# Kernel optimization log

Measured on AMD Instinct MI355X. Metric: run time of the kernel, lower is better.

The kernel has to match this reference:

```python
import jax, jax.numpy as jnp
import numpy as np

N = 50000   # num_entities
E = 600000  # num_edges
D = 128     # dim
R = 200     # num_relations
T = 1000    # num_timestamps
L = 2       # num_layers


def setup_inputs() -> dict:
    key = jax.random.key(0)
    ks = jax.random.split(key, 16)
    edge_index = jax.random.randint(ks[0], (2, E), 0, N)
    edge_type = jax.random.randint(ks[1], (E,), 0, R)
    edge_time = jax.random.randint(ks[2], (E,), 0, T)
    edge_weight = jax.random.uniform(ks[3], (E,), dtype=jnp.float32)
    perm = jax.random.permutation(ks[4], N)
    entity_emb = jax.random.normal(ks[5], (N, D), dtype=jnp.float32)
    rel_emb = jax.random.normal(ks[6], (R, D), dtype=jnp.float32)
    time_emb = jax.random.normal(ks[7], (T, D), dtype=jnp.float32)
    s = 1.0 / np.sqrt(D)
    in_proj_w = jax.random.uniform(ks[8], (L, D, 2 * D), minval=-s, maxval=s)
    in_proj_b = jax.random.uniform(ks[9], (L, 2 * D), minval=-s, maxval=s)
    out_proj_w = jax.random.uniform(ks[10], (L, D, D), minval=-s, maxval=s)
    out_proj_b = jax.random.uniform(ks[11], (L, D), minval=-s, maxval=s)
    A = jax.random.normal(ks[12], (L, D)) * 0.1
    B = jax.random.normal(ks[13], (L, D)) * 0.1
    ln_g = jnp.ones((L, D), dtype=jnp.float32)
    ln_b = jnp.zeros((L, D), dtype=jnp.float32)
    return dict(edge_index=edge_index, edge_type=edge_type, edge_time=edge_time,
                edge_weight=edge_weight, perm=perm, entity_emb=entity_emb,
                rel_emb=rel_emb, time_emb=time_emb, in_proj_w=in_proj_w,
                in_proj_b=in_proj_b, out_proj_w=out_proj_w, out_proj_b=out_proj_b,
                A=A, B=B, ln_g=ln_g, ln_b=ln_b)


def _mamba_layer(x, Wi, bi, Wo, bo, A, B, g_ln, b_ln):
    # x: [N, D]
    zg = x @ Wi + bi                      # [N, 2D]
    z, g = jnp.split(zg, 2, axis=-1)
    g = jax.nn.sigmoid(g)

    def step(prev, zg_i):
        z_i, g_i = zg_i
        curr = g_i * (A * prev) + B * z_i
        return curr, curr

    _, h = jax.lax.scan(step, jnp.zeros((D,), x.dtype), (z, g))  # [N, D]
    y = x + h @ Wo + bo
    mu = jnp.mean(y, axis=-1, keepdims=True)
    var = jnp.mean((y - mu) ** 2, axis=-1, keepdims=True)
    return (y - mu) / jnp.sqrt(var + 1e-5) * g_ln + b_ln


def reference(edge_index, edge_type, edge_time, edge_weight, perm, entity_emb,
              rel_emb, time_emb, in_proj_w, in_proj_b, out_proj_w, out_proj_b,
              A, B, ln_g, ln_b):
    src, dst = edge_index[0], edge_index[1]
    msgs = entity_emb[src] + rel_emb[edge_type] + time_emb[edge_time]  # [E, D]
    sums = jax.ops.segment_sum(msgs * edge_weight[:, None], dst, num_segments=N)
    cnt = jax.ops.segment_sum(edge_weight, dst, num_segments=N)
    x = sums / jnp.maximum(cnt, 1.0)[:, None]          # scatter_mean
    x = x / jnp.maximum(jnp.linalg.norm(x, axis=1, keepdims=True), 1e-12)
    x = x[perm]
    for l in range(L):
        x = _mamba_layer(x, in_proj_w[l], in_proj_b[l], out_proj_w[l],
                         out_proj_b[l], A[l], B[l], ln_g[l], ln_b[l])
    return x
```

## Files before the change

kernel.cpp:

```cpp
#include <hip/hip_runtime.h>
#include <hip/hip_bf16.h>

typedef unsigned short ushort_t;
typedef unsigned int   uint_t;
typedef __attribute__((ext_vector_type(8))) short bf8;
typedef __attribute__((ext_vector_type(4))) float f32x4;

constexpr int N = 50000;
constexpr int E = 600000;
constexpr int D = 128;
constexpr int L = 2;
constexpr int NB = (N + 255) / 256;

constexpr int TR   = 48;
constexpr int LOOK = 16;
constexpr int NBLK = (N + TR - 1) / TR;
constexpr int HSTR = 136;

__device__ __forceinline__ float us2f(ushort_t u) {
    union { uint_t i; float f; } c; c.i = (uint_t)u << 16; return c.f;
}
__device__ __forceinline__ ushort_t f2us(float f) {
    __hip_bfloat16 b = __float2bfloat16(f);
    return *(ushort_t*)&b;
}

__global__ __launch_bounds__(256) void k_hist(
    const int* __restrict__ dstp, int* __restrict__ hist)
{
    int e = blockIdx.x * 256 + threadIdx.x;
    if (e < E) atomicAdd(&hist[dstp[e]], 1);
}

__global__ __launch_bounds__(256) void k_scan1(
    const int* __restrict__ hist, int* __restrict__ part, int* __restrict__ bsum)
{
    int i = blockIdx.x * 256 + threadIdx.x;
    int v = (i < N) ? hist[i] : 0;
    int lane = threadIdx.x & 63, wv = threadIdx.x >> 6;
    int s = v;
    #pragma unroll
    for (int m = 1; m < 64; m <<= 1) {
        int t = __shfl_up(s, m, 64);
        if (lane >= m) s += t;
    }
    __shared__ int wsum[4];
    if (lane == 63) wsum[wv] = s;
    __syncthreads();
    int off = 0;
    for (int w = 0; w < wv; w++) off += wsum[w];
    if (i < N) part[i] = s - v + off;
    if (threadIdx.x == 255)
        bsum[blockIdx.x] = wsum[0] + wsum[1] + wsum[2] + wsum[3];
}

__global__ __launch_bounds__(256) void k_scan2(int* __restrict__ bsum)
{
    int i = threadIdx.x;
    int v = (i < NB) ? bsum[i] : 0;
    int lane = i & 63, wv = i >> 6;
    int s = v;
    #pragma unroll
    for (int m = 1; m < 64; m <<= 1) {
        int t = __shfl_up(s, m, 64);
        if (lane >= m) s += t;
    }
    __shared__ int wsum[4];
    if (lane == 63) wsum[wv] = s;
    __syncthreads();
    int off = 0;
    for (int w = 0; w < wv; w++) off += wsum[w];
    if (i < NB) bsum[i] = s - v + off;
}

__global__ __launch_bounds__(256) void k_finalize(
    const int* __restrict__ part, const int* __restrict__ bsum,
    int* __restrict__ cursor, int* __restrict__ rowst,
    const int* __restrict__ perm, int* __restrict__ invp)
{
    int i = blockIdx.x * 256 + threadIdx.x;
    if (i < N) {
        int b = part[i] + bsum[i >> 8];
        cursor[i] = b;
        rowst[i] = b;
        invp[perm[i]] = i;
    }
}

__global__ __launch_bounds__(256) void k_scatter(
    const int* __restrict__ eidx, const int* __restrict__ etype,
    const int* __restrict__ etime, const float* __restrict__ ew,
    int* __restrict__ cursor, int2* __restrict__ esort)
{
    int e = blockIdx.x * 256 + threadIdx.x;
    if (e >= E) return;
    int dst = eidx[E + e];
    int slot = atomicAdd(&cursor[dst], 1);
    int2 p;
    p.x = (eidx[e] & 0xffff) | (etype[e] << 16);
    p.y = (etime[e] & 0xffff) | ((int)f2us(ew[e]) << 16);
    esort[slot] = p;
}

__global__ __launch_bounds__(256) void k_cast(
    const float* __restrict__ ent, const float* __restrict__ rel,
    const float* __restrict__ tim, const float* __restrict__ Wi,
    const float* __restrict__ Wo, ushort_t* __restrict__ entb,
    ushort_t* __restrict__ relb, ushort_t* __restrict__ timb,
    ushort_t* __restrict__ WiT, ushort_t* __restrict__ WoT)
{
    size_t t = (size_t)blockIdx.x * 256 + threadIdx.x;
    if (t < 3276800) {
        const float2* s; uint_t* d; size_t off;
        if (t < 3200000)      { s = (const float2*)ent; d = (uint_t*)entb; off = t; }
        else if (t < 3212800) { s = (const float2*)rel; d = (uint_t*)relb; off = t - 3200000; }
        else                  { s = (const float2*)tim; d = (uint_t*)timb; off = t - 3212800; }
        float2 v = s[off];
        d[off] = (uint_t)f2us(v.x) | ((uint_t)f2us(v.y) << 16);
    } else {
        size_t u = t - 3276800;
        if (u < (size_t)L * 256 * 128) {
            int l = u / (256 * 128), r = u % (256 * 128);
            int n = r / 128, k = r % 128;
            WiT[u] = f2us(Wi[(size_t)l * 128 * 256 + k * 256 + n]);
        } else if (u < (size_t)L * 256 * 128 + L * 128 * 128) {
            size_t v = u - (size_t)L * 256 * 128;
            int l = v / (128 * 128), r = v % (128 * 128);
            int n = r / 128, k = r % 128;
            WoT[v] = f2us(Wo[(size_t)l * 128 * 128 + k * 128 + n]);
        }
    }
}

__global__ __launch_bounds__(256) void k_agg(
    const int2* __restrict__ esort, const int* __restrict__ rowst,
    const int* __restrict__ hist, const int* __restrict__ invp,
    const ushort_t* __restrict__ entb, const ushort_t* __restrict__ relb,
    const ushort_t* __restrict__ timb, ushort_t* __restrict__ xbf)
{
    int wv = threadIdx.x >> 6, lane = threadIdx.x & 63;
    int d = blockIdx.x * 4 + wv;
    if (d >= N) return;
    int beg = rowst[d];
    int n = hist[d];

    float s0[4] = {0.f, 0.f, 0.f, 0.f};
    float s1[4] = {0.f, 0.f, 0.f, 0.f};
    float sw[4] = {0.f, 0.f, 0.f, 0.f};

    int j = 0;
    for (; j + 3 < n; j += 4) {
        int2 rec[4];
        #pragma unroll
        for (int u = 0; u < 4; u++) rec[u] = esort[beg + j + u];
        #pragma unroll
        for (int u = 0; u < 4; u++) {
            int  sA = rec[u].x & 0xffff, tA = ((uint_t)rec[u].x) >> 16;
            int  mA = rec[u].y & 0xffff;
            float w = us2f((ushort_t)(((uint_t)rec[u].y) >> 16));
            uint_t va = *(const uint_t*)(entb + (size_t)sA * D + 2 * lane);
            uint_t vb = *(const uint_t*)(relb + (size_t)tA * D + 2 * lane);
            uint_t vc = *(const uint_t*)(timb + (size_t)mA * D + 2 * lane);
            s0[u] += (us2f(va & 0xffff) + us2f(vb & 0xffff) + us2f(vc & 0xffff)) * w;
            s1[u] += (us2f(va >> 16)    + us2f(vb >> 16)    + us2f(vc >> 16))    * w;
            sw[u] += w;
        }
    }
    for (; j < n; j++) {
        int2 p = esort[beg + j];
        int  sA = p.x & 0xffff, tA = ((uint_t)p.x) >> 16;
        int  mA = p.y & 0xffff;
        float w = us2f((ushort_t)(((uint_t)p.y) >> 16));
        uint_t va = *(const uint_t*)(entb + (size_t)sA * D + 2 * lane);
        uint_t vb = *(const uint_t*)(relb + (size_t)tA * D + 2 * lane);
        uint_t vc = *(const uint_t*)(timb + (size_t)mA * D + 2 * lane);
        s0[0] += (us2f(va & 0xffff) + us2f(vb & 0xffff) + us2f(vc & 0xffff)) * w;
        s1[0] += (us2f(va >> 16)    + us2f(vb >> 16)    + us2f(vc >> 16))    * w;
        sw[0] += w;
    }
    float a0 = (s0[0] + s0[1]) + (s0[2] + s0[3]);
    float a1 = (s1[0] + s1[1]) + (s1[2] + s1[3]);
    float wsum = (sw[0] + sw[1]) + (sw[2] + sw[3]);

    float inv = 1.0f / fmaxf(wsum, 1.0f);
    a0 *= inv; a1 *= inv;

    float ss = a0 * a0 + a1 * a1;
    #pragma unroll
    for (int m = 32; m >= 1; m >>= 1) ss += __shfl_xor(ss, m, 64);
    float sc = 1.0f / fmaxf(sqrtf(ss), 1e-12f);

    int orow = invp[d];
    uint_t out = (uint_t)f2us(a0 * sc) | ((uint_t)f2us(a1 * sc) << 16);
    *(uint_t*)(xbf + (size_t)orow * D + 2 * lane) = out;
}

template <bool FINAL>
__global__ __launch_bounds__(256, 4) void k_layer(
    const ushort_t* __restrict__ xin, const ushort_t* __restrict__ WiT,
    const float* __restrict__ bi, const ushort_t* __restrict__ WoT,
    const float* __restrict__ bo, const float* __restrict__ Aw,
    const float* __restrict__ Bw, const float* __restrict__ lg,
    const float* __restrict__ lb, ushort_t* __restrict__ xoutb,
    float* __restrict__ outf)
{
    __shared__ ushort_t hs[TR * HSTR];
    __shared__ float redS[TR * 4], redQ[TR * 4], muA[TR], rsA[TR];

    int tid = threadIdx.x;
    int w = tid >> 6, lane = tid & 63;
    int quad = lane >> 4, m = lane & 15;
    int r0 = blockIdx.x * TR;
    int base = r0 - LOOK;

    const bf8 zero8 = {0, 0, 0, 0, 0, 0, 0, 0};
    const f32x4 zero4 = {0.f, 0.f, 0.f, 0.f};

    int cz0 = w * 32 + m;
    int cz1 = cz0 + 16;

    float Ad0 = Aw[cz0], Bd0 = Bw[cz0];
    float Ad1 = Aw[cz1], Bd1 = Bw[cz1];
    float bz0 = bi[cz0], bz1 = bi[cz1];
    float bg0 = bi[cz0 + 128], bg1 = bi[cz1 + 128];

    bf8 Bz0[4], Bz1[4], Bg0[4], Bg1[4];
    {
        int colz0 = w * 32 + m, colz1 = colz0 + 16;
        #pragma unroll
        for (int kb = 0; kb < 4; kb++) {
            int ko = kb * 32 + quad * 8;
            Bz0[kb] = *(const bf8*)(WiT + (size_t)colz0 * 128 + ko);
            Bz1[kb] = *(const bf8*)(WiT + (size_t)colz1 * 128 + ko);
            Bg0[kb] = *(const bf8*)(WiT + (size_t)(colz0 + 128) * 128 + ko);
            Bg1[kb] = *(const bf8*)(WiT + (size_t)(colz1 + 128) * 128 + ko);
        }
    }

    float carry0 = 0.f, carry1 = 0.f;
    for (int rt = 0; rt < 4; rt++) {
        int gr = base + rt * 16 + m;
        bf8 a[4];
        if (gr >= 0 && gr < N) {
            #pragma unroll
            for (int kb = 0; kb < 4; kb++)
                a[kb] = *(const bf8*)(xin + (size_t)gr * 128 + kb * 32 + quad * 8);
        } else {
            #pragma unroll
            for (int kb = 0; kb < 4; kb++) a[kb] = zero8;
        }
        f32x4 az0 = zero4, az1 = zero4, ag0 = zero4, ag1 = zero4;
        #pragma unroll
        for (int kb = 0; kb < 4; kb++) {
            az0 = __builtin_amdgcn_mfma_f32_16x16x32_bf16(a[kb], Bz0[kb], az0, 0, 0, 0);
            az1 = __builtin_amdgcn_mfma_f32_16x16x32_bf16(a[kb], Bz1[kb], az1, 0, 0, 0);
            ag0 = __builtin_amdgcn_mfma_f32_16x16x32_bf16(a[kb], Bg0[kb], ag0, 0, 0, 0);
            ag1 = __builtin_amdgcn_mfma_f32_16x16x32_bf16(a[kb], Bg1[kb], ag1, 0, 0, 0);
        }
        float P0 = 1.f, Q0 = 0.f, P1 = 1.f, Q1 = 0.f;
        #pragma unroll
        for (int reg = 0; reg < 4; reg++) {
            int grr = base + rt * 16 + quad * 4 + reg;
            bool ok = (grr >= 0) && (grr < N);
            float z0 = az0[reg] + bz0, z1 = az1[reg] + bz1;
            float g0 = 1.f / (1.f + __expf(-(ag0[reg] + bg0)));
            float g1 = 1.f / (1.f + __expf(-(ag1[reg] + bg1)));
            float ca0 = ok ? g0 * Ad0 : 0.f, cb0 = ok ? Bd0 * z0 : 0.f;
            float ca1 = ok ? g1 * Ad1 : 0.f, cb1 = ok ? Bd1 * z1 : 0.f;
            az0[reg] = ca0; ag0[reg] = cb0;
            az1[reg] = ca1; ag1[reg] = cb1;
            P0 = ca0 * P0; Q0 = ca0 * Q0 + cb0;
            P1 = ca1 * P1; Q1 = ca1 * Q1 + cb1;
        }
        float Pp, Qp;
        Pp = __shfl_up(P0, 16, 64); Qp = __shfl_up(Q0, 16, 64);
        if (quad >= 1) { Q0 = P0 * Qp + Q0; P0 = P0 * Pp; }
        Pp = __shfl_up(P1, 16, 64); Qp = __shfl_up(Q1, 16, 64);
        if (quad >= 1) { Q1 = P1 * Qp + Q1; P1 = P1 * Pp; }
        Pp = __shfl_up(P0, 32, 64); Qp = __shfl_up(Q0, 32, 64);
        if (quad >= 2) { Q0 = P0 * Qp + Q0; P0 = P0 * Pp; }
        Pp = __shfl_up(P1, 32, 64); Qp = __shfl_up(Q1, 32, 64);
        if (quad >= 2) { Q1 = P1 * Qp + Q1; P1 = P1 * Pp; }
        float Pe0 = __shfl_up(P0, 16, 64), Qe0 = __shfl_up(Q0, 16, 64);
        float Pe1 = __shfl_up(P1, 16, 64), Qe1 = __shfl_up(Q1, 16, 64);
        if (quad == 0) { Pe0 = 1.f; Qe0 = 0.f; Pe1 = 1.f; Qe1 = 0.f; }
        float h0 = Pe0 * carry0 + Qe0;
        float h1 = Pe1 * carry1 + Qe1;
        float Pc0 = __shfl(P0, m + 48, 64), Qc0 = __shfl(Q0, m + 48, 64);
        float Pc1 = __shfl(P1, m + 48, 64), Qc1 = __shfl(Q1, m + 48, 64);
        carry0 = Pc0 * carry0 + Qc0;
        carry1 = Pc1 * carry1 + Qc1;
        #pragma unroll
        for (int reg = 0; reg < 4; reg++) {
            h0 = az0[reg] * h0 + ag0[reg];
            h1 = az1[reg] * h1 + ag1[reg];
            if (rt >= 1) {
                int lrow = (rt - 1) * 16 + quad * 4 + reg;
                hs[lrow * HSTR + cz0] = f2us(h0);
                hs[lrow * HSTR + cz1] = f2us(h1);
            }
        }
    }
    __syncthreads();

    float y[3][2][4];
    {
        int c0 = w * 32 + m, c1 = c0 + 16;
        float bias0 = bo[c0], bias1 = bo[c1];
        bf8 b0[4], b1[4];
        #pragma unroll
        for (int kb = 0; kb < 4; kb++) {
            int ko = kb * 32 + quad * 8;
            b0[kb] = *(const bf8*)(WoT + (size_t)c0 * 128 + ko);
            b1[kb] = *(const bf8*)(WoT + (size_t)c1 * 128 + ko);
        }
        #pragma unroll
        for (int rt = 0; rt < 3; rt++) {
            bf8 a[4];
            #pragma unroll
            for (int kb = 0; kb < 4; kb++)
                a[kb] = *(const bf8*)(hs + (rt * 16 + m) * HSTR + kb * 32 + quad * 8);
            f32x4 acc0 = zero4, acc1 = zero4;
            #pragma unroll
            for (int kb = 0; kb < 4; kb++) {
                acc0 = __builtin_amdgcn_mfma_f32_16x16x32_bf16(a[kb], b0[kb], acc0, 0, 0, 0);
                acc1 = __builtin_amdgcn_mfma_f32_16x16x32_bf16(a[kb], b1[kb], acc1, 0, 0, 0);
            }
            #pragma unroll
            for (int reg = 0; reg < 4; reg++) {
                int gr = r0 + rt * 16 + quad * 4 + reg;
                float r0v = 0.f, r1v = 0.f;
                if (gr < N) {
                    r0v = us2f(xin[(size_t)gr * 128 + c0]);
                    r1v = us2f(xin[(size_t)gr * 128 + c1]);
                }
                y[rt][0][reg] = acc0[reg] + bias0 + r0v;
                y[rt][1][reg] = acc1[reg] + bias1 + r1v;
            }
        }
    }

    {
        #pragma unroll
        for (int rt = 0; rt < 3; rt++)
            #pragma unroll
            for (int reg = 0; reg < 4; reg++) {
                float v0 = y[rt][0][reg], v1 = y[rt][1][reg];
                float s = v0 + v1, q = v0 * v0 + v1 * v1;
                #pragma unroll
                for (int mk = 1; mk <= 8; mk <<= 1) {
                    s += __shfl_xor(s, mk, 64);
                    q += __shfl_xor(q, mk, 64);
                }
                if (m == 0) {
                    int row = rt * 16 + quad * 4 + reg;
                    redS[row * 4 + w] = s;
                    redQ[row * 4 + w] = q;
                }
            }
    }
    __syncthreads();
    if (tid < TR) {
        float s = redS[tid * 4] + redS[tid * 4 + 1] + redS[tid * 4 + 2] + redS[tid * 4 + 3];
        float q = redQ[tid * 4] + redQ[tid * 4 + 1] + redQ[tid * 4 + 2] + redQ[tid * 4 + 3];
        float mu = s * (1.f / 128.f);
        float var = q * (1.f / 128.f) - mu * mu;
        muA[tid] = mu;
        rsA[tid] = rsqrtf(var + 1e-5f);
    }
    __syncthreads();
    {
        int c0 = w * 32 + m, c1 = c0 + 16;
        float gl0 = lg[c0], gl1 = lg[c1], bl0 = lb[c0], bl1 = lb[c1];
        #pragma unroll
        for (int rt = 0; rt < 3; rt++)
            #pragma unroll
            for (int reg = 0; reg < 4; reg++) {
                int rr = rt * 16 + quad * 4 + reg;
                int gr = r0 + rr;
                if (gr < N) {
                    float mu = muA[rr], rs = rsA[rr];
                    float v0 = (y[rt][0][reg] - mu) * rs * gl0 + bl0;
                    float v1 = (y[rt][1][reg] - mu) * rs * gl1 + bl1;
                    if (FINAL) {
                        outf[(size_t)gr * 128 + c0] = v0;
                        outf[(size_t)gr * 128 + c1] = v1;
                    } else {
                        xoutb[(size_t)gr * 128 + c0] = f2us(v0);
                        xoutb[(size_t)gr * 128 + c1] = f2us(v1);
                    }
                }
            }
    }
}

extern "C" void kernel_launch(void* const* d_in, const int* in_sizes, int n_in,
                              void* d_out, int out_size, void* d_ws, size_t ws_size,
                              hipStream_t stream)
{
    const int*   eidx  = (const int*)d_in[0];
    const int*   etype = (const int*)d_in[1];
    const int*   etime = (const int*)d_in[2];
    const float* ew    = (const float*)d_in[3];
    const int*   perm  = (const int*)d_in[4];
    const float* ent   = (const float*)d_in[5];
    const float* rel   = (const float*)d_in[6];
    const float* tim   = (const float*)d_in[7];
    const float* Wi    = (const float*)d_in[8];
    const float* bi    = (const float*)d_in[9];
    const float* Wo    = (const float*)d_in[10];
    const float* bo    = (const float*)d_in[11];
    const float* Aw    = (const float*)d_in[12];
    const float* Bw    = (const float*)d_in[13];
    const float* lg    = (const float*)d_in[14];
    const float* lbp   = (const float*)d_in[15];

    char* base = (char*)d_ws;
    size_t o = 0;
    ushort_t* xbf  = (ushort_t*)(base + o); o += (size_t)N * D * 2;
    ushort_t* xb2  = (ushort_t*)(base + o); o += (size_t)N * D * 2;
    ushort_t* entb = (ushort_t*)(base + o); o += (size_t)N * D * 2;
    ushort_t* relb = (ushort_t*)(base + o); o += (size_t)200 * D * 2;
    ushort_t* timb = (ushort_t*)(base + o); o += (size_t)1000 * D * 2;
    ushort_t* WiT  = (ushort_t*)(base + o); o += (size_t)L * 256 * 128 * 2;
    ushort_t* WoT  = (ushort_t*)(base + o); o += (size_t)L * 128 * 128 * 2;
    int2*     esort  = (int2*)(base + o);   o += (size_t)E * 8;
    int*      hist   = (int*)(base + o);    o += (size_t)N * 4;
    int*      part   = (int*)(base + o);    o += (size_t)N * 4;
    int*      bsum   = (int*)(base + o);    o += 256 * 4;
    int*      cursor = (int*)(base + o);    o += (size_t)N * 4;
    int*      rowst  = (int*)(base + o);    o += (size_t)N * 4;
    int*      invp   = (int*)(base + o);    o += (size_t)N * 4;

    hipMemsetAsync(hist, 0, N * sizeof(int), stream);

    k_cast    <<<13185, 256, 0, stream>>>(ent, rel, tim, Wi, Wo,
                                          entb, relb, timb, WiT, WoT);
    k_hist    <<<(E + 255) / 256, 256, 0, stream>>>(eidx + E, hist);
    k_scan1   <<<NB, 256, 0, stream>>>(hist, part, bsum);
    k_scan2   <<<1, 256, 0, stream>>>(bsum);
    k_finalize<<<NB, 256, 0, stream>>>(part, bsum, cursor, rowst, perm, invp);
    k_scatter <<<(E + 255) / 256, 256, 0, stream>>>(eidx, etype, etime, ew,
                                                    cursor, esort);
    k_agg     <<<(N + 3) / 4, 256, 0, stream>>>(esort, rowst, hist, invp,
                                                entb, relb, timb, xbf);

    k_layer<false><<<NBLK, 256, 0, stream>>>(
        xbf, WiT, bi, WoT, bo, Aw, Bw, lg, lbp, xb2, nullptr);
    k_layer<true><<<NBLK, 256, 0, stream>>>(
        xb2, WiT + (size_t)256 * 128, bi + 256, WoT + (size_t)128 * 128,
        bo + 128, Aw + 128, Bw + 128, lg + 128, lbp + 128,
        nullptr, (float*)d_out);
}
```

Baseline: 304.6 us.

## Split mamba layer into coefficient GEMM kernel and scan+output kernel

Each layer is split into two kernels. The first computes the gate and z projections once per row and stores packed bf16 scan coefficients to global memory. The second runs a sequential lookback scan over those coefficients per channel with 128 threads, then applies the out-projection, residual and layernorm on 16-row blocks. This removes the redundant lookback GEMM that the fused 48-row tiles did, at the cost of an extra global round trip for the coefficient buffer, two extra launches, and a serial scan with few active threads.

```diff
diff --git a/kernel.cpp b/kernel.cpp
--- a/kernel.cpp
+++ b/kernel.cpp
@@ -12,9 +12,9 @@
 constexpr int L = 2;
 constexpr int NB = (N + 255) / 256;
 
-constexpr int TR   = 48;
+constexpr int RB   = 16;
+constexpr int RBLK = N / RB;
 constexpr int LOOK = 16;
-constexpr int NBLK = (N + TR - 1) / TR;
 constexpr int HSTR = 136;
 
 __device__ __forceinline__ float us2f(ushort_t u) {
@@ -195,26 +195,15 @@
     *(uint_t*)(xbf + (size_t)orow * D + 2 * lane) = out;
 }
 
-template <bool FINAL>
-__global__ __launch_bounds__(256, 4) void k_layer(
+__global__ __launch_bounds__(256, 4) void k_zg(
     const ushort_t* __restrict__ xin, const ushort_t* __restrict__ WiT,
-    const float* __restrict__ bi, const ushort_t* __restrict__ WoT,
-    const float* __restrict__ bo, const float* __restrict__ Aw,
-    const float* __restrict__ Bw, const float* __restrict__ lg,
-    const float* __restrict__ lb, ushort_t* __restrict__ xoutb,
-    float* __restrict__ outf)
-{
-    __shared__ ushort_t hs[TR * HSTR];
-    __shared__ float redS[TR * 4], redQ[TR * 4], muA[TR], rsA[TR];
-
+    const float* __restrict__ bi, const float* __restrict__ Aw,
+    const float* __restrict__ Bw, uint_t* __restrict__ coeff)
+{
     int tid = threadIdx.x;
     int w = tid >> 6, lane = tid & 63;
     int quad = lane >> 4, m = lane & 15;
-    int r0 = blockIdx.x * TR;
-    int base = r0 - LOOK;
-
-    const bf8 zero8 = {0, 0, 0, 0, 0, 0, 0, 0};
-    const f32x4 zero4 = {0.f, 0.f, 0.f, 0.f};
+    int r0 = blockIdx.x * RB;
 
     int cz0 = w * 32 + m;
     int cz1 = cz0 + 16;
@@ -224,143 +213,139 @@
     float bz0 = bi[cz0], bz1 = bi[cz1];
     float bg0 = bi[cz0 + 128], bg1 = bi[cz1 + 128];
 
+    const f32x4 zero4 = {0.f, 0.f, 0.f, 0.f};
+
     bf8 Bz0[4], Bz1[4], Bg0[4], Bg1[4];
+    #pragma unroll
+    for (int kb = 0; kb < 4; kb++) {
+        int ko = kb * 32 + quad * 8;
+        Bz0[kb] = *(const bf8*)(WiT + (size_t)cz0 * 128 + ko);
+        Bz1[kb] = *(const bf8*)(WiT + (size_t)cz1 * 128 + ko);
+        Bg0[kb] = *(const bf8*)(WiT + (size_t)(cz0 + 128) * 128 + ko);
+        Bg1[kb] = *(const bf8*)(WiT + (size_t)(cz1 + 128) * 128 + ko);
+    }
+
+    bf8 a[4];
+    #pragma unroll
+    for (int kb = 0; kb < 4; kb++)
+        a[kb] = *(const bf8*)(xin + (size_t)(r0 + m) * 128 + kb * 32 + quad * 8);
+
+    f32x4 az0 = zero4, az1 = zero4, ag0 = zero4, ag1 = zero4;
+    #pragma unroll
+    for (int kb = 0; kb < 4; kb++) {
+        az0 = __builtin_amdgcn_mfma_f32_16x16x32_bf16(a[kb], Bz0[kb], az0, 0, 0, 0);
+        az1 = __builtin_amdgcn_mfma_f32_16x16x32_bf16(a[kb], Bz1[kb], az1, 0, 0, 0);
+        ag0 = __builtin_amdgcn_mfma_f32_16x16x32_bf16(a[kb], Bg0[kb], ag0, 0, 0, 0);
+        ag1 = __builtin_amdgcn_mfma_f32_16x16x32_bf16(a[kb], Bg1[kb], ag1, 0, 0, 0);
+    }
+
+    #pragma unroll
+    for (int reg = 0; reg < 4; reg++) {
+        int row = r0 + quad * 4 + reg;
+        float z0 = az0[reg] + bz0, z1 = az1[reg] + bz1;
+        float g0 = 1.f / (1.f + __expf(-(ag0[reg] + bg0)));
+        float g1 = 1.f / (1.f + __expf(-(ag1[reg] + bg1)));
+        uint_t c0 = (uint_t)f2us(g0 * Ad0) | ((uint_t)f2us(Bd0 * z0) << 16);
+        uint_t c1 = (uint_t)f2us(g1 * Ad1) | ((uint_t)f2us(Bd1 * z1) << 16);
+        coeff[(size_t)row * 128 + cz0] = c0;
+        coeff[(size_t)row * 128 + cz1] = c1;
+    }
+}
+
+template <bool FINAL>
+__global__ __launch_bounds__(256, 4) void k_scanout(
+    const uint_t* __restrict__ coeff, const ushort_t* __restrict__ xin,
+    const ushort_t* __restrict__ WoT, const float* __restrict__ bo,
+    const float* __restrict__ lg, const float* __restrict__ lb,
+    ushort_t* __restrict__ xoutb, float* __restrict__ outf)
+{
+    __shared__ ushort_t hs[RB * HSTR];
+    __shared__ float redS[RB * 4], redQ[RB * 4], muA[RB], rsA[RB];
+
+    int tid = threadIdx.x;
+    int w = tid >> 6, lane = tid & 63;
+    int quad = lane >> 4, m = lane & 15;
+    int r0 = blockIdx.x * RB;
+
+    int c0 = w * 32 + m, c1 = c0 + 16;
+
+    bf8 b0[4], b1[4];
+    #pragma unroll
+    for (int kb = 0; kb < 4; kb++) {
+        int ko = kb * 32 + quad * 8;
+        b0[kb] = *(const bf8*)(WoT + (size_t)c0 * 128 + ko);
+        b1[kb] = *(const bf8*)(WoT + (size_t)c1 * 128 + ko);
+    }
+    float bias0 = bo[c0], bias1 = bo[c1];
+    float gl0 = lg[c0], gl1 = lg[c1], bl0 = lb[c0], bl1 = lb[c1];
+
+    float r0v[4], r1v[4];
+    #pragma unroll
+    for (int reg = 0; reg < 4; reg++) {
+        int gr = r0 + quad * 4 + reg;
+        r0v[reg] = us2f(xin[(size_t)gr * 128 + c0]);
+        r1v[reg] = us2f(xin[(size_t)gr * 128 + c1]);
+    }
+
+    if (tid < 128) {
+        float h = 0.f;
+        int rbase = r0 - LOOK;
+        #pragma unroll
+        for (int i = 0; i < LOOK; i++) {
+            int row = rbase + i;
+            int rc = row < 0 ? 0 : row;
+            uint_t c = coeff[(size_t)rc * 128 + tid];
+            float ca = us2f((ushort_t)(c & 0xffff));
+            float cb = us2f((ushort_t)(c >> 16));
+            h = (row >= 0) ? fmaf(ca, h, cb) : 0.f;
+        }
+        #pragma unroll
+        for (int i = 0; i < RB; i++) {
+            uint_t c = coeff[(size_t)(r0 + i) * 128 + tid];
+            float ca = us2f((ushort_t)(c & 0xffff));
+            float cb = us2f((ushort_t)(c >> 16));
+            h = fmaf(ca, h, cb);
+            hs[i * HSTR + tid] = f2us(h);
+        }
+    }
+    __syncthreads();
+
+    float y[2][4];
     {
-        int colz0 = w * 32 + m, colz1 = colz0 + 16;
+        bf8 a[4];
+        #pragma unroll
+        for (int kb = 0; kb < 4; kb++)
+            a[kb] = *(const bf8*)(hs + m * HSTR + kb * 32 + quad * 8);
+        f32x4 acc0 = {0.f, 0.f, 0.f, 0.f}, acc1 = acc0;
         #pragma unroll
         for (int kb = 0; kb < 4; kb++) {
-            int ko = kb * 32 + quad * 8;
-            Bz0[kb] = *(const bf8*)(WiT + (size_t)colz0 * 128 + ko);
-            Bz1[kb] = *(const bf8*)(WiT + (size_t)colz1 * 128 + ko);
-            Bg0[kb] = *(const bf8*)(WiT + (size_t)(colz0 + 128) * 128 + ko);
-            Bg1[kb] = *(const bf8*)(WiT + (size_t)(colz1 + 128) * 128 + ko);
-        }
-    }
-
-    float carry0 = 0.f, carry1 = 0.f;
-    for (int rt = 0; rt < 4; rt++) {
-        int gr = base + rt * 16 + m;
-        bf8 a[4];
-        if (gr >= 0 && gr < N) {
-            #pragma unroll
-            for (int kb = 0; kb < 4; kb++)
-                a[kb] = *(const bf8*)(xin + (size_t)gr * 128 + kb * 32 + quad * 8);
-        } else {
-            #pragma unroll
-            for (int kb = 0; kb < 4; kb++) a[kb] = zero8;
-        }
-        f32x4 az0 = zero4, az1 = zero4, ag0 = zero4, ag1 = zero4;
-        #pragma unroll
-        for (int kb = 0; kb < 4; kb++) {
-            az0 = __builtin_amdgcn_mfma_f32_16x16x32_bf16(a[kb], Bz0[kb], az0, 0, 0, 0);
-            az1 = __builtin_amdgcn_mfma_f32_16x16x32_bf16(a[kb], Bz1[kb], az1, 0, 0, 0);
-            ag0 = __builtin_amdgcn_mfma_f32_16x16x32_bf16(a[kb], Bg0[kb], ag0, 0, 0, 0);
-            ag1 = __builtin_amdgcn_mfma_f32_16x16x32_bf16(a[kb], Bg1[kb], ag1, 0, 0, 0);
-        }
-        float P0 = 1.f, Q0 = 0.f, P1 = 1.f, Q1 = 0.f;
+            acc0 = __builtin_amdgcn_mfma_f32_16x16x32_bf16(a[kb], b0[kb], acc0, 0, 0, 0);
+            acc1 = __builtin_amdgcn_mfma_f32_16x16x32_bf16(a[kb], b1[kb], acc1, 0, 0, 0);
+        }
         #pragma unroll
         for (int reg = 0; reg < 4; reg++) {
-            int grr = base + rt * 16 + quad * 4 + reg;
-            bool ok = (grr >= 0) && (grr < N);
-            float z0 = az0[reg] + bz0, z1 = az1[reg] + bz1;
-            float g0 = 1.f / (1.f + __expf(-(ag0[reg] + bg0)));
-            float g1 = 1.f / (1.f + __expf(-(ag1[reg] + bg1)));
-            float ca0 = ok ? g0 * Ad0 : 0.f, cb0 = ok ? Bd0 * z0 : 0.f;
-            float ca1 = ok ? g1 * Ad1 : 0.f, cb1 = ok ? Bd1 * z1 : 0.f;
-            az0[reg] = ca0; ag0[reg] = cb0;
-            az1[reg] = ca1; ag1[reg] = cb1;
-            P0 = ca0 * P0; Q0 = ca0 * Q0 + cb0;
-            P1 = ca1 * P1; Q1 = ca1 * Q1 + cb1;
-        }
-        float Pp, Qp;
-        Pp = __shfl_up(P0, 16, 64); Qp = __shfl_up(Q0, 16, 64);
-        if (quad >= 1) { Q0 = P0 * Qp + Q0; P0 = P0 * Pp; }
-        Pp = __shfl_up(P1, 16, 64); Qp = __shfl_up(Q1, 16, 64);
-        if (quad >= 1) { Q1 = P1 * Qp + Q1; P1 = P1 * Pp; }
-        Pp = __shfl_up(P0, 32, 64); Qp = __shfl_up(Q0, 32, 64);
-        if (quad >= 2) { Q0 = P0 * Qp + Q0; P0 = P0 * Pp; }
-        Pp = __shfl_up(P1, 32, 64); Qp = __shfl_up(Q1, 32, 64);
-        if (quad >= 2) { Q1 = P1 * Qp + Q1; P1 = P1 * Pp; }
-        float Pe0 = __shfl_up(P0, 16, 64), Qe0 = __shfl_up(Q0, 16, 64);
-        float Pe1 = __shfl_up(P1, 16, 64), Qe1 = __shfl_up(Q1, 16, 64);
-        if (quad == 0) { Pe0 = 1.f; Qe0 = 0.f; Pe1 = 1.f; Qe1 = 0.f; }
-        float h0 = Pe0 * carry0 + Qe0;
-        float h1 = Pe1 * carry1 + Qe1;
-        float Pc0 = __shfl(P0, m + 48, 64), Qc0 = __shfl(Q0, m + 48, 64);
-        float Pc1 = __shfl(P1, m + 48, 64), Qc1 = __shfl(Q1, m + 48, 64);
-        carry0 = Pc0 * carry0 + Qc0;
-        carry1 = Pc1 * carry1 + Qc1;
-        #pragma unroll
-        for (int reg = 0; reg < 4; reg++) {
-            h0 = az0[reg] * h0 + ag0[reg];
-            h1 = az1[reg] * h1 + ag1[reg];
-            if (rt >= 1) {
-                int lrow = (rt - 1) * 16 + quad * 4 + reg;
-                hs[lrow * HSTR + cz0] = f2us(h0);
-                hs[lrow * HSTR + cz1] = f2us(h1);
-            }
+            y[0][reg] = acc0[reg] + bias0 + r0v[reg];
+            y[1][reg] = acc1[reg] + bias1 + r1v[reg];
+        }
+    }
+
+    #pragma unroll
+    for (int reg = 0; reg < 4; reg++) {
+        float v0 = y[0][reg], v1 = y[1][reg];
+        float s = v0 + v1, q = v0 * v0 + v1 * v1;
+        #pragma unroll
+        for (int mk = 1; mk <= 8; mk <<= 1) {
+            s += __shfl_xor(s, mk, 64);
+            q += __shfl_xor(q, mk, 64);
+        }
+        if (m == 0) {
+            int row = quad * 4 + reg;
+            redS[row * 4 + w] = s;
+            redQ[row * 4 + w] = q;
         }
     }
     __syncthreads();
-
-    float y[3][2][4];
-    {
-        int c0 = w * 32 + m, c1 = c0 + 16;
-        float bias0 = bo[c0], bias1 = bo[c1];
-        bf8 b0[4], b1[4];
-        #pragma unroll
-        for (int kb = 0; kb < 4; kb++) {
-            int ko = kb * 32 + quad * 8;
-            b0[kb] = *(const bf8*)(WoT + (size_t)c0 * 128 + ko);
-            b1[kb] = *(const bf8*)(WoT + (size_t)c1 * 128 + ko);
-        }
-        #pragma unroll
-        for (int rt = 0; rt < 3; rt++) {
-            bf8 a[4];
-            #pragma unroll
-            for (int kb = 0; kb < 4; kb++)
-                a[kb] = *(const bf8*)(hs + (rt * 16 + m) * HSTR + kb * 32 + quad * 8);
-            f32x4 acc0 = zero4, acc1 = zero4;
-            #pragma unroll
-            for (int kb = 0; kb < 4; kb++) {
-                acc0 = __builtin_amdgcn_mfma_f32_16x16x32_bf16(a[kb], b0[kb], acc0, 0, 0, 0);
-                acc1 = __builtin_amdgcn_mfma_f32_16x16x32_bf16(a[kb], b1[kb], acc1, 0, 0, 0);
-            }
-            #pragma unroll
-            for (int reg = 0; reg < 4; reg++) {
-                int gr = r0 + rt * 16 + quad * 4 + reg;
-                float r0v = 0.f, r1v = 0.f;
-                if (gr < N) {
-                    r0v = us2f(xin[(size_t)gr * 128 + c0]);
-                    r1v = us2f(xin[(size_t)gr * 128 + c1]);
-                }
-                y[rt][0][reg] = acc0[reg] + bias0 + r0v;
-                y[rt][1][reg] = acc1[reg] + bias1 + r1v;
-            }
-        }
-    }
-
-    {
-        #pragma unroll
-        for (int rt = 0; rt < 3; rt++)
-            #pragma unroll
-            for (int reg = 0; reg < 4; reg++) {
-                float v0 = y[rt][0][reg], v1 = y[rt][1][reg];
-                float s = v0 + v1, q = v0 * v0 + v1 * v1;
-                #pragma unroll
-                for (int mk = 1; mk <= 8; mk <<= 1) {
-                    s += __shfl_xor(s, mk, 64);
-                    q += __shfl_xor(q, mk, 64);
-                }
-                if (m == 0) {
-                    int row = rt * 16 + quad * 4 + reg;
-                    redS[row * 4 + w] = s;
-                    redQ[row * 4 + w] = q;
-                }
-            }
-    }
-    __syncthreads();
-    if (tid < TR) {
+    if (tid < RB) {
         float s = redS[tid * 4] + redS[tid * 4 + 1] + redS[tid * 4 + 2] + redS[tid * 4 + 3];
         float q = redQ[tid * 4] + redQ[tid * 4 + 1] + redQ[tid * 4 + 2] + redQ[tid * 4 + 3];
         float mu = s * (1.f / 128.f);
@@ -369,28 +354,20 @@
         rsA[tid] = rsqrtf(var + 1e-5f);
     }
     __syncthreads();
-    {
-        int c0 = w * 32 + m, c1 = c0 + 16;
-        float gl0 = lg[c0], gl1 = lg[c1], bl0 = lb[c0], bl1 = lb[c1];
-        #pragma unroll
-        for (int rt = 0; rt < 3; rt++)
-            #pragma unroll
-            for (int reg = 0; reg < 4; reg++) {
-                int rr = rt * 16 + quad * 4 + reg;
-                int gr = r0 + rr;
-                if (gr < N) {
-                    float mu = muA[rr], rs = rsA[rr];
-                    float v0 = (y[rt][0][reg] - mu) * rs * gl0 + bl0;
-                    float v1 = (y[rt][1][reg] - mu) * rs * gl1 + bl1;
-                    if (FINAL) {
-                        outf[(size_t)gr * 128 + c0] = v0;
-                        outf[(size_t)gr * 128 + c1] = v1;
-                    } else {
-                        xoutb[(size_t)gr * 128 + c0] = f2us(v0);
-                        xoutb[(size_t)gr * 128 + c1] = f2us(v1);
-                    }
-                }
-            }
+    #pragma unroll
+    for (int reg = 0; reg < 4; reg++) {
+        int rr = quad * 4 + reg;
+        int gr = r0 + rr;
+        float mu = muA[rr], rs = rsA[rr];
+        float v0 = (y[0][reg] - mu) * rs * gl0 + bl0;
+        float v1 = (y[1][reg] - mu) * rs * gl1 + bl1;
+        if (FINAL) {
+            outf[(size_t)gr * 128 + c0] = v0;
+            outf[(size_t)gr * 128 + c1] = v1;
+        } else {
+            xoutb[(size_t)gr * 128 + c0] = f2us(v0);
+            xoutb[(size_t)gr * 128 + c1] = f2us(v1);
+        }
     }
 }
 
@@ -431,6 +408,7 @@
     int*      cursor = (int*)(base + o);    o += (size_t)N * 4;
     int*      rowst  = (int*)(base + o);    o += (size_t)N * 4;
     int*      invp   = (int*)(base + o);    o += (size_t)N * 4;
+    uint_t*   coeff  = (uint_t*)(base + o); o += (size_t)N * D * 4;
 
     hipMemsetAsync(hist, 0, N * sizeof(int), stream);
 
@@ -445,10 +423,13 @@
     k_agg     <<<(N + 3) / 4, 256, 0, stream>>>(esort, rowst, hist, invp,
                                                 entb, relb, timb, xbf);
 
-    k_layer<false><<<NBLK, 256, 0, stream>>>(
-        xbf, WiT, bi, WoT, bo, Aw, Bw, lg, lbp, xb2, nullptr);
-    k_layer<true><<<NBLK, 256, 0, stream>>>(
-        xb2, WiT + (size_t)256 * 128, bi + 256, WoT + (size_t)128 * 128,
-        bo + 128, Aw + 128, Bw + 128, lg + 128, lbp + 128,
-        nullptr, (float*)d_out);
-}
+    k_zg<<<RBLK, 256, 0, stream>>>(xbf, WiT, bi, Aw, Bw, coeff);
+    k_scanout<false><<<RBLK, 256, 0, stream>>>(coeff, xbf, WoT, bo, lg, lbp,
+                                               xb2, nullptr);
+    k_zg<<<RBLK, 256, 0, stream>>>(xb2, WiT + (size_t)256 * 128, bi + 256,
+                                   Aw + 128, Bw + 128, coeff);
+    k_scanout<true><<<RBLK, 256, 0, stream>>>(coeff, xb2,
+                                              WoT + (size_t)128 * 128, bo + 128,
+                                              lg + 128, lbp + 128,
+                                              nullptr, (float*)d_out);
+}
```

After: 363.3 us. 19.3% more time.
